# Performance work log

Hardware: AMD Instinct MI355X
Metric: run time of the kernel (lower is better)

## Reference

```python
import jax, jax.numpy as jnp
import numpy as np

TOP_K = 2


def setup_inputs() -> dict:
    key = jax.random.key(0)
    ks = jax.random.split(key, 6)
    B, S, H, I, E = 2, 1024, 1024, 2048, 8
    s_h = 1.0 / np.sqrt(H)
    s_i = 1.0 / np.sqrt(I)
    return {
        "x": jax.random.normal(ks[0], (B, S, H), jnp.float32),
        "gate_w": jax.random.normal(ks[1], (H, E), jnp.float32) * s_h,
        "gate_b": jnp.zeros((E,), jnp.float32),
        "w1": jax.random.normal(ks[2], (E, H, I), jnp.float32) * s_h,
        "w3": jax.random.normal(ks[3], (E, H, I), jnp.float32) * s_h,
        "w2": jax.random.normal(ks[4], (E, I, H), jnp.float32) * s_i,
    }


def reference(x, gate_w, gate_b, w1, w3, w2):
    # Gating: softmax over experts, then top-k selection + renormalization.
    logits = jnp.einsum("bsh,he->bse", x, gate_w) + gate_b            # [B,S,E]
    probs = jax.nn.softmax(logits, axis=-1)
    topk_w, topk_idx = jax.lax.top_k(probs, TOP_K)                    # [B,S,K]
    topk_w = topk_w / jnp.sum(topk_w, axis=-1, keepdims=True)

    E = gate_w.shape[-1]
    # Per-token combine weight for each expert (0 if not routed there).
    # one_hot: [B,S,K,E] -> combine: [B,S,E]
    combine = jnp.sum(jax.nn.one_hot(topk_idx, E, dtype=x.dtype) * topk_w[..., None], axis=-2)

    # SwiGLU expert FFN: down(silu(gate(x)) * up(x)); dense-masked reference
    # (compute every expert on every token, weight by combine; math identical
    # to the original gather/scatter loop since combine is 0 off-route).
    out = jnp.zeros_like(x)
    for e in range(E):
        h = jax.nn.silu(x @ w1[e]) * (x @ w3[e])                      # [B,S,I]
        out = out + combine[..., e:e + 1] * (h @ w2[e])               # [B,S,H]
    return out
```

## Files before the change

kernel.cpp:

```cpp
#include <hip/hip_runtime.h>
#include <hip/hip_bf16.h>
#include <math.h>

typedef __attribute__((ext_vector_type(4))) float f32x4;
typedef __attribute__((ext_vector_type(8))) short bf16x8;

#define T_TOK 2048
#define H_DIM 1024
#define I_DIM 2048
#define E_NUM 8

__device__ inline unsigned short f2bf(float f) {
  union { float f; unsigned int u; } v; v.f = f;
  unsigned int r = v.u + 0x7fffu + ((v.u >> 16) & 1u);
  return (unsigned short)(r >> 16);
}
__device__ inline unsigned int pack2(float a, float b) {
  return (unsigned int)f2bf(a) | ((unsigned int)f2bf(b) << 16);
}

__device__ inline void gld16(const void* g, void* l) {
  __builtin_amdgcn_global_load_lds((const __attribute__((address_space(1))) void*)g,
                                   (__attribute__((address_space(3))) void*)l, 16, 0, 0);
}

__device__ inline void transpose256(const float* __restrict__ ip, unsigned short* __restrict__ op,
                                    int R, int C, int rp, int ct, char* smem)
{
  unsigned short (*tl)[264] = (unsigned short (*)[264])smem;
  int r0 = rp * 256, c0 = ct * 128;
  int tid = threadIdx.x;
  int cg = tid & 31;
  int rg = tid >> 5;
  int S = 8 * (cg & 7);

  const float* base = ip + (size_t)(r0 + rg * 4) * C + c0 + cg * 4;
#pragma unroll
  for (int p = 0; p < 8; ++p) {
    const float* bp = base + (size_t)(p * 32) * C;
    float4 v0 = *(const float4*)(bp);
    float4 v1 = *(const float4*)(bp + C);
    float4 v2 = *(const float4*)(bp + 2 * C);
    float4 v3 = *(const float4*)(bp + 3 * C);
    int rr = p * 32 + rg * 4;
    int rph = rr ^ S;
#pragma unroll
    for (int j = 0; j < 4; ++j) {
      *(unsigned int*)&tl[cg * 4 + j][rph]     = pack2(v0[j], v1[j]);
      *(unsigned int*)&tl[cg * 4 + j][rph + 2] = pack2(v2[j], v3[j]);
    }
  }
  __syncthreads();
  int cs = tid >> 5;
  int rs = (tid & 31) * 8;
#pragma unroll
  for (int cc = 0; cc < 16; ++cc) {
    int c = cc * 8 + cs;
    int Sc = 8 * ((c >> 2) & 7);
    uint4 o = *(const uint4*)&tl[c][rs ^ Sc];
    *(uint4*)(op + (size_t)(c0 + c) * R + r0 + rs) = o;
  }
}

__global__ __launch_bounds__(256) void gate_t13(
    const float* __restrict__ x, const float* __restrict__ gw, const float* __restrict__ gb,
    int* __restrict__ rec_e, float* __restrict__ rec_w, unsigned short* __restrict__ xb,
    const float* __restrict__ w1, const float* __restrict__ w3,
    unsigned short* __restrict__ w1t, unsigned short* __restrict__ w3t,
    const float* __restrict__ w2, unsigned short* __restrict__ w2t)
{
  __shared__ __align__(16) char smem[128 * 264 * 2];
  int bx = blockIdx.x;
  if (bx >= 1536) {
    int idx = bx - 1536;
    int e = idx >> 6;
    int sub = idx & 63;
    int rp = sub & 7;
    int ct = sub >> 3;
    const float* ip = w2 + (size_t)e * ((size_t)H_DIM * I_DIM);
    unsigned short* op = w2t + (size_t)e * ((size_t)H_DIM * I_DIM);
    transpose256(ip, op, I_DIM, H_DIM, rp, ct, smem);
    return;
  }
  if (bx >= 512) {
    int idx = bx - 512;
    int m = idx >> 6;
    int sub = idx & 63;
    int rp = sub & 3;
    int ct = sub >> 2;
    const float* ip = (m < 8 ? w1 : w3) + (size_t)(m & 7) * ((size_t)H_DIM * I_DIM);
    unsigned short* op = (m < 8 ? w1t : w3t) + (size_t)(m & 7) * ((size_t)H_DIM * I_DIM);
    transpose256(ip, op, H_DIM, I_DIM, rp, ct, smem);
    return;
  }
  int wv = threadIdx.x >> 6, lane = threadIdx.x & 63;
  int t = bx * 4 + wv;
  const float* xr = x + (size_t)t * H_DIM;
  unsigned short* xo = xb + (size_t)t * H_DIM;
  float acc[8];
#pragma unroll
  for (int e = 0; e < 8; ++e) acc[e] = 0.f;
  for (int i = 0; i < H_DIM / 64; ++i) {
    int h = i * 64 + lane;
    float xv = xr[h];
    xo[h] = f2bf(xv);
    const float4* g = (const float4*)(gw + (size_t)h * 8);
    float4 g0 = g[0], g1 = g[1];
    acc[0] += xv * g0.x; acc[1] += xv * g0.y; acc[2] += xv * g0.z; acc[3] += xv * g0.w;
    acc[4] += xv * g1.x; acc[5] += xv * g1.y; acc[6] += xv * g1.z; acc[7] += xv * g1.w;
  }
#pragma unroll
  for (int s = 1; s < 64; s <<= 1) {
#pragma unroll
    for (int e = 0; e < 8; ++e) acc[e] += __shfl_xor(acc[e], s);
  }
  if (lane == 0) {
    float l[8];
#pragma unroll
    for (int e = 0; e < 8; ++e) l[e] = acc[e] + gb[e];
    int e0 = 0;
    for (int e = 1; e < 8; ++e) if (l[e] > l[e0]) e0 = e;
    int e1 = (e0 == 0) ? 1 : 0;
    for (int e = 0; e < 8; ++e) if (e != e0 && l[e] > l[e1]) e1 = e;
    float w0 = 1.f / (1.f + expf(l[e1] - l[e0]));
    rec_e[t * 2]     = e0; rec_e[t * 2 + 1] = e1;
    rec_w[t * 2]     = w0; rec_w[t * 2 + 1] = 1.f - w0;
  }
}

__global__ __launch_bounds__(256) void route8(
    const int* __restrict__ rec_e, const float* __restrict__ rec_w,
    int* __restrict__ counts_g, int* __restrict__ list_tok, float* __restrict__ list_w)
{
  __shared__ int cnt[8];
  __shared__ int fill;
  int e = blockIdx.x;
  int tid = threadIdx.x;
  if (tid < 8) cnt[tid] = 0;
  if (tid == 0) fill = 0;
  __syncthreads();
  int e_loc[16];
  int c_loc[8];
#pragma unroll
  for (int k = 0; k < 8; ++k) c_loc[k] = 0;
#pragma unroll
  for (int it = 0; it < 16; ++it) {
    e_loc[it] = rec_e[it * 256 + tid] & 7;
    c_loc[e_loc[it]]++;
  }
#pragma unroll
  for (int k = 0; k < 8; ++k) if (c_loc[k]) atomicAdd(&cnt[k], c_loc[k]);
  __syncthreads();
  if (e == 0 && tid < 8) counts_g[tid] = cnt[tid];
  int base = 0;
#pragma unroll
  for (int k = 0; k < 8; ++k) if (k < e) base += cnt[k];
#pragma unroll
  for (int it = 0; it < 16; ++it) {
    if (e_loc[it] == e) {
      int i = it * 256 + tid;
      int pos = atomicAdd(&fill, 1);
      list_tok[base + pos] = i;
      list_w[base + pos]   = rec_w[i];
    }
  }
}

__global__ __launch_bounds__(256, 2) void gemm1(
    const unsigned short* __restrict__ xb,
    const unsigned short* __restrict__ w1t,
    const unsigned short* __restrict__ w3t,
    const int* __restrict__ counts,
    const int* __restrict__ list_tok,
    unsigned short* __restrict__ hbuf)
{
  __shared__ __align__(16) char smem[49152];
  int bx = blockIdx.x;
  int e = bx >> 9;
  int y = (bx >> 4) & 31;
  int ix = bx & 15;
  int nbase = 0;
#pragma unroll
  for (int i = 0; i < 8; ++i) if (i < e) nbase += counts[i];
  int n_e = counts[e];
  int t0 = y * 128;
  if (t0 >= n_e) return;
  int i0 = ix * 128;

  int tid = threadIdx.x;
  int r2 = tid >> 2;
  int sseg = (((tid & 3) ^ (r2 & 3)) * 8);

  int sr0 = t0 + r2;       if (sr0 >= n_e) sr0 = n_e - 1;
  int sr1 = t0 + 64 + r2;  if (sr1 >= n_e) sr1 = n_e - 1;
  int tok0 = list_tok[nbase + sr0] >> 1;
  int tok1 = list_tok[nbase + sr1] >> 1;
  const char* gA0  = (const char*)(xb + (size_t)tok0 * H_DIM + sseg);
  const char* gA1  = (const char*)(xb + (size_t)tok1 * H_DIM + sseg);
  const char* gB1a = (const char*)(w1t + ((size_t)e * I_DIM + i0 + r2) * H_DIM + sseg);
  const char* gB1b = (const char*)(w1t + ((size_t)e * I_DIM + i0 + 64 + r2) * H_DIM + sseg);
  const char* gB3a = (const char*)(w3t + ((size_t)e * I_DIM + i0 + r2) * H_DIM + sseg);
  const char* gB3b = (const char*)(w3t + ((size_t)e * I_DIM + i0 + 64 + r2) * H_DIM + sseg);

#define STAGE1(buf, kb) do {                              \
    gld16(gA0  + (kb) * 2, (buf) + tid * 16);             \
    gld16(gA1  + (kb) * 2, (buf) + 4096  + tid * 16);     \
    gld16(gB1a + (kb) * 2, (buf) + 8192  + tid * 16);     \
    gld16(gB1b + (kb) * 2, (buf) + 12288 + tid * 16);     \
    gld16(gB3a + (kb) * 2, (buf) + 16384 + tid * 16);     \
    gld16(gB3b + (kb) * 2, (buf) + 20480 + tid * 16);     \
  } while (0)

  int w = tid >> 6, lane = tid & 63, lm = lane & 15, lq = lane >> 4;
  int wm = w & 1, wn = w >> 1;
  int colx = (lq ^ (lm & 3)) * 16;
  int rA = (wm * 64 + lm) * 64 + colx;
  int rB = (wn * 64 + lm) * 64 + colx;

  f32x4 acc1[4][4], acc3[4][4];
#pragma unroll
  for (int i = 0; i < 4; ++i)
#pragma unroll
    for (int j = 0; j < 4; ++j) { acc1[i][j] = (f32x4){0,0,0,0}; acc3[i][j] = (f32x4){0,0,0,0}; }

  STAGE1(smem, 0);
  __syncthreads();
  for (int kb = 0; kb < H_DIM; kb += 32) {
    char* cur = smem + (((kb >> 5) & 1) ? 24576 : 0);
    char* nxt = smem + (((kb >> 5) & 1) ? 0 : 24576);
    if (kb + 32 < H_DIM) STAGE1(nxt, kb + 32);
    bf16x8 a[4], b1[4], b3[4];
#pragma unroll
    for (int i = 0; i < 4; ++i)
      a[i] = *(const bf16x8*)(cur + rA + i * 1024);
#pragma unroll
    for (int j = 0; j < 4; ++j) {
      b1[j] = *(const bf16x8*)(cur + 8192  + rB + j * 1024);
      b3[j] = *(const bf16x8*)(cur + 16384 + rB + j * 1024);
    }
#pragma unroll
    for (int i = 0; i < 4; ++i)
#pragma unroll
      for (int j = 0; j < 4; ++j) {
        acc1[i][j] = __builtin_amdgcn_mfma_f32_16x16x32_bf16(a[i], b1[j], acc1[i][j], 0, 0, 0);
        acc3[i][j] = __builtin_amdgcn_mfma_f32_16x16x32_bf16(a[i], b3[j], acc3[i][j], 0, 0, 0);
      }
    __syncthreads();
  }
#undef STAGE1

#pragma unroll
  for (int i = 0; i < 4; ++i) {
#pragma unroll
    for (int rr = 0; rr < 4; ++rr) {
      int slot = t0 + wm * 64 + i * 16 + lq * 4 + rr;
      if (slot < n_e) {
        unsigned short* orow = hbuf + (size_t)(nbase + slot) * I_DIM + i0 + wn * 64 + lm;
#pragma unroll
        for (int j = 0; j < 4; ++j) {
          float g = acc1[i][j][rr], u = acc3[i][j][rr];
          float hv = (g / (1.f + __expf(-g))) * u;
          orow[j * 16] = f2bf(hv);
        }
      }
    }
  }
}

__global__ __launch_bounds__(256, 4) void gemm2(
    const unsigned short* __restrict__ hbuf,
    const unsigned short* __restrict__ w2t,
    const int* __restrict__ counts,
    const int* __restrict__ list_tok,
    const float* __restrict__ list_w,
    float* __restrict__ partial)
{
  __shared__ __align__(16) char smem[24576];
  int e = blockIdx.z;
  int nbase = 0;
#pragma unroll
  for (int i = 0; i < 8; ++i) if (i < e) nbase += counts[i];
  int n_e = counts[e];
  int ts = blockIdx.y >> 1, kh = blockIdx.y & 1;
  int t0 = ts * 64;
  if (t0 >= n_e) return;
  int h0 = blockIdx.x * 128;
  int k0 = kh * (I_DIM / 2);

  int tid = threadIdx.x;
  int r2 = tid >> 2;
  int sseg = (((tid & 3) ^ (r2 & 3)) * 8);

  int sr = t0 + r2; if (sr >= n_e) sr = n_e - 1;
  const char* gA  = (const char*)(hbuf + (size_t)(nbase + sr) * I_DIM + k0 + sseg);
  const char* gB0 = (const char*)(w2t + ((size_t)e * H_DIM + h0 + r2) * I_DIM + k0 + sseg);
  const char* gB1 = (const char*)(w2t + ((size_t)e * H_DIM + h0 + 64 + r2) * I_DIM + k0 + sseg);

#define STAGE2(buf, kb) do {                              \
    gld16(gA  + (kb) * 2, (buf) + tid * 16);              \
    gld16(gB0 + (kb) * 2, (buf) + 4096 + tid * 16);       \
    gld16(gB1 + (kb) * 2, (buf) + 8192 + tid * 16);       \
  } while (0)

  int w = tid >> 6, lane = tid & 63, lm = lane & 15, lq = lane >> 4;
  int wm = w & 1, wn = w >> 1;
  int colx = (lq ^ (lm & 3)) * 16;
  int rA = (wm * 32 + lm) * 64 + colx;
  int rB = (wn * 64 + lm) * 64 + colx;

  f32x4 acc[2][4];
#pragma unroll
  for (int i = 0; i < 2; ++i)
#pragma unroll
    for (int j = 0; j < 4; ++j) acc[i][j] = (f32x4){0,0,0,0};

  STAGE2(smem, 0);
  __syncthreads();
  for (int kb = 0; kb < I_DIM / 2; kb += 32) {
    char* cur = smem + (((kb >> 5) & 1) ? 12288 : 0);
    char* nxt = smem + (((kb >> 5) & 1) ? 0 : 12288);
    if (kb + 32 < I_DIM / 2) STAGE2(nxt, kb + 32);
    bf16x8 a[2], b[4];
#pragma unroll
    for (int i = 0; i < 2; ++i)
      a[i] = *(const bf16x8*)(cur + rA + i * 1024);
#pragma unroll
    for (int j = 0; j < 4; ++j)
      b[j] = *(const bf16x8*)(cur + 4096 + rB + j * 1024);
#pragma unroll
    for (int i = 0; i < 2; ++i)
#pragma unroll
      for (int j = 0; j < 4; ++j)
        acc[i][j] = __builtin_amdgcn_mfma_f32_16x16x32_bf16(a[i], b[j], acc[i][j], 0, 0, 0);
    __syncthreads();
  }
#undef STAGE2

  int entv[2][4]; float wtv[2][4];
#pragma unroll
  for (int i = 0; i < 2; ++i)
#pragma unroll
    for (int rr = 0; rr < 4; ++rr) {
      int slot = t0 + wm * 32 + i * 16 + lq * 4 + rr;
      if (slot < n_e) { entv[i][rr] = list_tok[nbase + slot]; wtv[i][rr] = list_w[nbase + slot]; }
      else entv[i][rr] = -1;
    }
#pragma unroll
  for (int i = 0; i < 2; ++i)
#pragma unroll
    for (int j = 0; j < 4; ++j)
#pragma unroll
      for (int rr = 0; rr < 4; ++rr) {
        if (entv[i][rr] >= 0) {
          int t = entv[i][rr] >> 1, kk = entv[i][rr] & 1;
          int plane = kh * 2 + kk;
          partial[((size_t)plane * T_TOK + t) * H_DIM + h0 + wn * 64 + j * 16 + lm] =
              acc[i][j][rr] * wtv[i][rr];
        }
      }
}

__global__ __launch_bounds__(256) void combine4(const float* __restrict__ partial,
                                                float* __restrict__ out)
{
  const size_t P = (size_t)T_TOK * H_DIM;
  size_t i = (size_t)(blockIdx.x * 256 + threadIdx.x) * 4;
  float4 a = *(const float4*)(partial + i);
  float4 b = *(const float4*)(partial + P + i);
  float4 c = *(const float4*)(partial + 2 * P + i);
  float4 d = *(const float4*)(partial + 3 * P + i);
  float4 o;
  o.x = a.x + b.x + c.x + d.x;
  o.y = a.y + b.y + c.y + d.y;
  o.z = a.z + b.z + c.z + d.z;
  o.w = a.w + b.w + c.w + d.w;
  *(float4*)(out + i) = o;
}

extern "C" void kernel_launch(void* const* d_in, const int* in_sizes, int n_in,
                              void* d_out, int out_size, void* d_ws, size_t ws_size,
                              hipStream_t stream) {
  const float* x  = (const float*)d_in[0];
  const float* gw = (const float*)d_in[1];
  const float* gb = (const float*)d_in[2];
  const float* w1 = (const float*)d_in[3];
  const float* w3 = (const float*)d_in[4];
  const float* w2 = (const float*)d_in[5];
  float* out = (float*)d_out;

  char* ws = (char*)d_ws;
  int*   counts   = (int*)(ws);
  int*   rec_e    = (int*)(ws + 128);
  float* rec_w    = (float*)(ws + 16512);
  int*   list_tok = (int*)(ws + 32896);
  float* list_w   = (float*)(ws + 49280);
  const size_t MB = 1024ull * 1024ull;
  unsigned short* xb   = (unsigned short*)(ws + 1 * MB);
  unsigned short* w1t  = (unsigned short*)(ws + 5 * MB);
  float* partial       = (float*)(ws + 5 * MB);
  unsigned short* w3t  = (unsigned short*)(ws + 37 * MB);
  unsigned short* w2t  = (unsigned short*)(ws + 69 * MB);
  unsigned short* hbuf = (unsigned short*)(ws + 101 * MB);

  gate_t13<<<2048, 256, 0, stream>>>(x, gw, gb, rec_e, rec_w, xb,
                                     w1, w3, w1t, w3t, w2, w2t);
  route8<<<8, 256, 0, stream>>>(rec_e, rec_w, counts, list_tok, list_w);
  gemm1<<<4096, 256, 0, stream>>>(xb, w1t, w3t, counts, list_tok, hbuf);
  gemm2<<<dim3(H_DIM / 128, 128, E_NUM), 256, 0, stream>>>(hbuf, w2t, counts, list_tok, list_w, partial);
  combine4<<<(T_TOK * H_DIM) / (256 * 4), 256, 0, stream>>>(partial, out);
}
```

Baseline: 359.7 us.

## Fuse fp32 weight conversion and transpose into GEMM B-tile staging

Drops the separate pre-pass that converted and transposed w1, w3 and w2 to bf16 in workspace. Each GEMM now loads fp32 weight rows into registers one stage ahead, packs them to bf16 with v_cvt_pk_bf16_f32, and writes them transposed into a swizzled LDS layout; the B-fragment reads use a matching per-column swizzle. This removes the full-weight read, write and re-read round trip through HBM. In exchange the GEMMs read twice as many weight bytes per tile, repeat that read for every token tile, and use register-staged loads with more VALU and LDS-store work in the main loop.

Result: faster. 347.1 us (-3.5%).

```diff
diff --git a/kernel.cpp b/kernel.cpp
--- a/kernel.cpp
+++ b/kernel.cpp
@@ -15,8 +15,11 @@
   unsigned int r = v.u + 0x7fffu + ((v.u >> 16) & 1u);
   return (unsigned short)(r >> 16);
 }
-__device__ inline unsigned int pack2(float a, float b) {
-  return (unsigned int)f2bf(a) | ((unsigned int)f2bf(b) << 16);
+
+__device__ inline unsigned int cvtpk(float a, float b) {
+  unsigned int r;
+  asm("v_cvt_pk_bf16_f32 %0, %1, %2" : "=v"(r) : "v"(a), "v"(b));
+  return r;
 }
 
 __device__ inline void gld16(const void* g, void* l) {
@@ -24,77 +27,12 @@
                                    (__attribute__((address_space(3))) void*)l, 16, 0, 0);
 }
 
-__device__ inline void transpose256(const float* __restrict__ ip, unsigned short* __restrict__ op,
-                                    int R, int C, int rp, int ct, char* smem)
-{
-  unsigned short (*tl)[264] = (unsigned short (*)[264])smem;
-  int r0 = rp * 256, c0 = ct * 128;
-  int tid = threadIdx.x;
-  int cg = tid & 31;
-  int rg = tid >> 5;
-  int S = 8 * (cg & 7);
-
-  const float* base = ip + (size_t)(r0 + rg * 4) * C + c0 + cg * 4;
-#pragma unroll
-  for (int p = 0; p < 8; ++p) {
-    const float* bp = base + (size_t)(p * 32) * C;
-    float4 v0 = *(const float4*)(bp);
-    float4 v1 = *(const float4*)(bp + C);
-    float4 v2 = *(const float4*)(bp + 2 * C);
-    float4 v3 = *(const float4*)(bp + 3 * C);
-    int rr = p * 32 + rg * 4;
-    int rph = rr ^ S;
-#pragma unroll
-    for (int j = 0; j < 4; ++j) {
-      *(unsigned int*)&tl[cg * 4 + j][rph]     = pack2(v0[j], v1[j]);
-      *(unsigned int*)&tl[cg * 4 + j][rph + 2] = pack2(v2[j], v3[j]);
-    }
-  }
-  __syncthreads();
-  int cs = tid >> 5;
-  int rs = (tid & 31) * 8;
-#pragma unroll
-  for (int cc = 0; cc < 16; ++cc) {
-    int c = cc * 8 + cs;
-    int Sc = 8 * ((c >> 2) & 7);
-    uint4 o = *(const uint4*)&tl[c][rs ^ Sc];
-    *(uint4*)(op + (size_t)(c0 + c) * R + r0 + rs) = o;
-  }
-}
-
-__global__ __launch_bounds__(256) void gate_t13(
+__global__ __launch_bounds__(256) void gate_k(
     const float* __restrict__ x, const float* __restrict__ gw, const float* __restrict__ gb,
-    int* __restrict__ rec_e, float* __restrict__ rec_w, unsigned short* __restrict__ xb,
-    const float* __restrict__ w1, const float* __restrict__ w3,
-    unsigned short* __restrict__ w1t, unsigned short* __restrict__ w3t,
-    const float* __restrict__ w2, unsigned short* __restrict__ w2t)
-{
-  __shared__ __align__(16) char smem[128 * 264 * 2];
-  int bx = blockIdx.x;
-  if (bx >= 1536) {
-    int idx = bx - 1536;
-    int e = idx >> 6;
-    int sub = idx & 63;
-    int rp = sub & 7;
-    int ct = sub >> 3;
-    const float* ip = w2 + (size_t)e * ((size_t)H_DIM * I_DIM);
-    unsigned short* op = w2t + (size_t)e * ((size_t)H_DIM * I_DIM);
-    transpose256(ip, op, I_DIM, H_DIM, rp, ct, smem);
-    return;
-  }
-  if (bx >= 512) {
-    int idx = bx - 512;
-    int m = idx >> 6;
-    int sub = idx & 63;
-    int rp = sub & 3;
-    int ct = sub >> 2;
-    const float* ip = (m < 8 ? w1 : w3) + (size_t)(m & 7) * ((size_t)H_DIM * I_DIM);
-    unsigned short* op = (m < 8 ? w1t : w3t) + (size_t)(m & 7) * ((size_t)H_DIM * I_DIM);
-    transpose256(ip, op, H_DIM, I_DIM, rp, ct, smem);
-    return;
-  }
+    int* __restrict__ rec_e, float* __restrict__ rec_w, unsigned short* __restrict__ xb)
+{
   int wv = threadIdx.x >> 6, lane = threadIdx.x & 63;
-  int t = bx * 4 + wv;
+  int t = blockIdx.x * 4 + wv;
   const float* xr = x + (size_t)t * H_DIM;
   unsigned short* xo = xb + (size_t)t * H_DIM;
   float acc[8];
@@ -168,8 +106,8 @@
 
 __global__ __launch_bounds__(256, 2) void gemm1(
     const unsigned short* __restrict__ xb,
-    const unsigned short* __restrict__ w1t,
-    const unsigned short* __restrict__ w3t,
+    const float* __restrict__ w1,
+    const float* __restrict__ w3,
     const int* __restrict__ counts,
     const int* __restrict__ list_tok,
     unsigned short* __restrict__ hbuf)
@@ -195,27 +133,47 @@
   int sr1 = t0 + 64 + r2;  if (sr1 >= n_e) sr1 = n_e - 1;
   int tok0 = list_tok[nbase + sr0] >> 1;
   int tok1 = list_tok[nbase + sr1] >> 1;
-  const char* gA0  = (const char*)(xb + (size_t)tok0 * H_DIM + sseg);
-  const char* gA1  = (const char*)(xb + (size_t)tok1 * H_DIM + sseg);
-  const char* gB1a = (const char*)(w1t + ((size_t)e * I_DIM + i0 + r2) * H_DIM + sseg);
-  const char* gB1b = (const char*)(w1t + ((size_t)e * I_DIM + i0 + 64 + r2) * H_DIM + sseg);
-  const char* gB3a = (const char*)(w3t + ((size_t)e * I_DIM + i0 + r2) * H_DIM + sseg);
-  const char* gB3b = (const char*)(w3t + ((size_t)e * I_DIM + i0 + 64 + r2) * H_DIM + sseg);
-
-#define STAGE1(buf, kb) do {                              \
-    gld16(gA0  + (kb) * 2, (buf) + tid * 16);             \
-    gld16(gA1  + (kb) * 2, (buf) + 4096  + tid * 16);     \
-    gld16(gB1a + (kb) * 2, (buf) + 8192  + tid * 16);     \
-    gld16(gB1b + (kb) * 2, (buf) + 12288 + tid * 16);     \
-    gld16(gB3a + (kb) * 2, (buf) + 16384 + tid * 16);     \
-    gld16(gB3b + (kb) * 2, (buf) + 20480 + tid * 16);     \
+  const char* gA0 = (const char*)(xb + (size_t)tok0 * H_DIM + sseg);
+  const char* gA1 = (const char*)(xb + (size_t)tok1 * H_DIM + sseg);
+
+#define STAGEA1(buf, kb) do {                             \
+    gld16(gA0 + (kb) * 2, (buf) + tid * 16);              \
+    gld16(gA1 + (kb) * 2, (buf) + 4096 + tid * 16);       \
+  } while (0)
+
+  int gq = tid >> 5, lif = tid & 31;
+  const float* pB1 = w1 + (size_t)e * ((size_t)H_DIM * I_DIM) + (size_t)(gq * 4) * I_DIM + i0 + lif * 4;
+  const float* pB3 = w3 + (size_t)e * ((size_t)H_DIM * I_DIM) + (size_t)(gq * 4) * I_DIM + i0 + lif * 4;
+  int wb = (lif * 4) * 64 + (((gq >> 1) ^ ((lif >> 1) & 3)) * 16) + (gq & 1) * 8;
+
+  float4 v0, v1, v2, v3, q0, q1, q2, q3;
+#define LOADB1(kb) do {                                                        \
+    const float* p1 = pB1 + (size_t)(kb) * I_DIM;                              \
+    const float* p3 = pB3 + (size_t)(kb) * I_DIM;                              \
+    v0 = *(const float4*)(p1);             v1 = *(const float4*)(p1 + I_DIM);  \
+    v2 = *(const float4*)(p1 + 2 * I_DIM); v3 = *(const float4*)(p1 + 3 * I_DIM); \
+    q0 = *(const float4*)(p3);             q1 = *(const float4*)(p3 + I_DIM);  \
+    q2 = *(const float4*)(p3 + 2 * I_DIM); q3 = *(const float4*)(p3 + 3 * I_DIM); \
+  } while (0)
+#define WRITEB1(buf) do {                                                      \
+    char* c1 = (buf) + 8192 + wb; char* c3 = (buf) + 16384 + wb;               \
+    _Pragma("unroll") for (int k = 0; k < 4; ++k) {                            \
+      uint2 d1; d1.x = cvtpk(v0[k], v1[k]); d1.y = cvtpk(v2[k], v3[k]);        \
+      uint2 d3; d3.x = cvtpk(q0[k], q1[k]); d3.y = cvtpk(q2[k], q3[k]);        \
+      *(uint2*)(c1 + k * 64) = d1;                                             \
+      *(uint2*)(c3 + k * 64) = d3;                                             \
+    }                                                                          \
   } while (0)
 
   int w = tid >> 6, lane = tid & 63, lm = lane & 15, lq = lane >> 4;
   int wm = w & 1, wn = w >> 1;
-  int colx = (lq ^ (lm & 3)) * 16;
-  int rA = (wm * 64 + lm) * 64 + colx;
-  int rB = (wn * 64 + lm) * 64 + colx;
+  int lmh = lm >> 3;
+  int colA = (lq ^ (lm & 3)) * 16;
+  int rA = (wm * 64 + lm) * 64 + colA;
+  int rBb = (wn * 64 + lm) * 64;
+  int cb[4];
+#pragma unroll
+  for (int j = 0; j < 4; ++j) cb[j] = (lq ^ ((j * 2 + lmh) & 3)) * 16;
 
   f32x4 acc1[4][4], acc3[4][4];
 #pragma unroll
@@ -223,21 +181,26 @@
 #pragma unroll
     for (int j = 0; j < 4; ++j) { acc1[i][j] = (f32x4){0,0,0,0}; acc3[i][j] = (f32x4){0,0,0,0}; }
 
-  STAGE1(smem, 0);
+  LOADB1(0);
+  STAGEA1(smem, 0);
+  WRITEB1(smem);
+  LOADB1(32);
   __syncthreads();
-  for (int kb = 0; kb < H_DIM; kb += 32) {
-    char* cur = smem + (((kb >> 5) & 1) ? 24576 : 0);
-    char* nxt = smem + (((kb >> 5) & 1) ? 0 : 24576);
-    if (kb + 32 < H_DIM) STAGE1(nxt, kb + 32);
+  for (int t = 0; t < 32; ++t) {
+    char* cur = smem + (t & 1) * 24576;
+    char* nxt = smem + ((t + 1) & 1) * 24576;
+    if (t < 31) STAGEA1(nxt, (t + 1) * 32);
     bf16x8 a[4], b1[4], b3[4];
 #pragma unroll
     for (int i = 0; i < 4; ++i)
       a[i] = *(const bf16x8*)(cur + rA + i * 1024);
 #pragma unroll
     for (int j = 0; j < 4; ++j) {
-      b1[j] = *(const bf16x8*)(cur + 8192  + rB + j * 1024);
-      b3[j] = *(const bf16x8*)(cur + 16384 + rB + j * 1024);
+      b1[j] = *(const bf16x8*)(cur + 8192  + rBb + j * 1024 + cb[j]);
+      b3[j] = *(const bf16x8*)(cur + 16384 + rBb + j * 1024 + cb[j]);
     }
+    if (t < 31) WRITEB1(nxt);
+    if (t < 30) LOADB1((t + 2) * 32);
 #pragma unroll
     for (int i = 0; i < 4; ++i)
 #pragma unroll
@@ -247,7 +210,9 @@
       }
     __syncthreads();
   }
-#undef STAGE1
+#undef STAGEA1
+#undef LOADB1
+#undef WRITEB1
 
 #pragma unroll
   for (int i = 0; i < 4; ++i) {
@@ -269,7 +234,7 @@
 
 __global__ __launch_bounds__(256, 4) void gemm2(
     const unsigned short* __restrict__ hbuf,
-    const unsigned short* __restrict__ w2t,
+    const float* __restrict__ w2,
     const int* __restrict__ counts,
     const int* __restrict__ list_tok,
     const float* __restrict__ list_w,
@@ -292,21 +257,37 @@
   int sseg = (((tid & 3) ^ (r2 & 3)) * 8);
 
   int sr = t0 + r2; if (sr >= n_e) sr = n_e - 1;
-  const char* gA  = (const char*)(hbuf + (size_t)(nbase + sr) * I_DIM + k0 + sseg);
-  const char* gB0 = (const char*)(w2t + ((size_t)e * H_DIM + h0 + r2) * I_DIM + k0 + sseg);
-  const char* gB1 = (const char*)(w2t + ((size_t)e * H_DIM + h0 + 64 + r2) * I_DIM + k0 + sseg);
-
-#define STAGE2(buf, kb) do {                              \
-    gld16(gA  + (kb) * 2, (buf) + tid * 16);              \
-    gld16(gB0 + (kb) * 2, (buf) + 4096 + tid * 16);       \
-    gld16(gB1 + (kb) * 2, (buf) + 8192 + tid * 16);       \
+  const char* gA = (const char*)(hbuf + (size_t)(nbase + sr) * I_DIM + k0 + sseg);
+
+#define STAGEA2(buf, kb) do { gld16(gA + (kb) * 2, (buf) + tid * 16); } while (0)
+
+  int gq = tid >> 5, lif = tid & 31;
+  const float* pB = w2 + (size_t)e * ((size_t)H_DIM * I_DIM) + (size_t)(k0 + gq * 4) * H_DIM + h0 + lif * 4;
+  int wb = (lif * 4) * 64 + (((gq >> 1) ^ ((lif >> 1) & 3)) * 16) + (gq & 1) * 8;
+
+  float4 v0, v1, v2, v3;
+#define LOADB2(kb) do {                                                        \
+    const float* p = pB + (size_t)(kb) * H_DIM;                                \
+    v0 = *(const float4*)(p);             v1 = *(const float4*)(p + H_DIM);    \
+    v2 = *(const float4*)(p + 2 * H_DIM); v3 = *(const float4*)(p + 3 * H_DIM); \
+  } while (0)
+#define WRITEB2(buf) do {                                                      \
+    char* c = (buf) + 4096 + wb;                                               \
+    _Pragma("unroll") for (int k = 0; k < 4; ++k) {                            \
+      uint2 d; d.x = cvtpk(v0[k], v1[k]); d.y = cvtpk(v2[k], v3[k]);           \
+      *(uint2*)(c + k * 64) = d;                                               \
+    }                                                                          \
   } while (0)
 
   int w = tid >> 6, lane = tid & 63, lm = lane & 15, lq = lane >> 4;
   int wm = w & 1, wn = w >> 1;
-  int colx = (lq ^ (lm & 3)) * 16;
-  int rA = (wm * 32 + lm) * 64 + colx;
-  int rB = (wn * 64 + lm) * 64 + colx;
+  int lmh = lm >> 3;
+  int colA = (lq ^ (lm & 3)) * 16;
+  int rA = (wm * 32 + lm) * 64 + colA;
+  int rBb = (wn * 64 + lm) * 64;
+  int cb[4];
+#pragma unroll
+  for (int j = 0; j < 4; ++j) cb[j] = (lq ^ ((j * 2 + lmh) & 3)) * 16;
 
   f32x4 acc[2][4];
 #pragma unroll
@@ -314,19 +295,24 @@
 #pragma unroll
     for (int j = 0; j < 4; ++j) acc[i][j] = (f32x4){0,0,0,0};
 
-  STAGE2(smem, 0);
+  LOADB2(0);
+  STAGEA2(smem, 0);
+  WRITEB2(smem);
+  LOADB2(32);
   __syncthreads();
-  for (int kb = 0; kb < I_DIM / 2; kb += 32) {
-    char* cur = smem + (((kb >> 5) & 1) ? 12288 : 0);
-    char* nxt = smem + (((kb >> 5) & 1) ? 0 : 12288);
-    if (kb + 32 < I_DIM / 2) STAGE2(nxt, kb + 32);
+  for (int t = 0; t < 32; ++t) {
+    char* cur = smem + (t & 1) * 12288;
+    char* nxt = smem + ((t + 1) & 1) * 12288;
+    if (t < 31) STAGEA2(nxt, (t + 1) * 32);
     bf16x8 a[2], b[4];
 #pragma unroll
     for (int i = 0; i < 2; ++i)
       a[i] = *(const bf16x8*)(cur + rA + i * 1024);
 #pragma unroll
     for (int j = 0; j < 4; ++j)
-      b[j] = *(const bf16x8*)(cur + 4096 + rB + j * 1024);
+      b[j] = *(const bf16x8*)(cur + 4096 + rBb + j * 1024 + cb[j]);
+    if (t < 31) WRITEB2(nxt);
+    if (t < 30) LOADB2((t + 2) * 32);
 #pragma unroll
     for (int i = 0; i < 2; ++i)
 #pragma unroll
@@ -334,7 +320,9 @@
         acc[i][j] = __builtin_amdgcn_mfma_f32_16x16x32_bf16(a[i], b[j], acc[i][j], 0, 0, 0);
     __syncthreads();
   }
-#undef STAGE2
+#undef STAGEA2
+#undef LOADB2
+#undef WRITEB2
 
   int entv[2][4]; float wtv[2][4];
 #pragma unroll
@@ -395,17 +383,13 @@
   int*   list_tok = (int*)(ws + 32896);
   float* list_w   = (float*)(ws + 49280);
   const size_t MB = 1024ull * 1024ull;
-  unsigned short* xb   = (unsigned short*)(ws + 1 * MB);
-  unsigned short* w1t  = (unsigned short*)(ws + 5 * MB);
-  float* partial       = (float*)(ws + 5 * MB);
-  unsigned short* w3t  = (unsigned short*)(ws + 37 * MB);
-  unsigned short* w2t  = (unsigned short*)(ws + 69 * MB);
+  unsigned short* xb = (unsigned short*)(ws + 1 * MB);
+  float* partial     = (float*)(ws + 5 * MB);
   unsigned short* hbuf = (unsigned short*)(ws + 101 * MB);
 
-  gate_t13<<<2048, 256, 0, stream>>>(x, gw, gb, rec_e, rec_w, xb,
-                                     w1, w3, w1t, w3t, w2, w2t);
+  gate_k<<<512, 256, 0, stream>>>(x, gw, gb, rec_e, rec_w, xb);
   route8<<<8, 256, 0, stream>>>(rec_e, rec_w, counts, list_tok, list_w);
-  gemm1<<<4096, 256, 0, stream>>>(xb, w1t, w3t, counts, list_tok, hbuf);
-  gemm2<<<dim3(H_DIM / 128, 128, E_NUM), 256, 0, stream>>>(hbuf, w2t, counts, list_tok, list_w, partial);
+  gemm1<<<4096, 256, 0, stream>>>(xb, w1, w3, counts, list_tok, hbuf);
+  gemm2<<<dim3(H_DIM / 128, 128, E_NUM), 256, 0, stream>>>(hbuf, w2, counts, list_tok, list_w, partial);
   combine4<<<(T_TOK * H_DIM) / (256 * 4), 256, 0, stream>>>(partial, out);
 }
```
